# Kernel tuning notes

Hardware: AMD Instinct MI355X
Metric: run time of the kernel (lower is better)

The kernel has to match this reference:

```python
import jax, jax.numpy as jnp
import numpy as np

B, N_REG, D_IN = 32, 116, 256
N_NODES = B * N_REG            # 3712
E_PER_G = N_REG * 10           # avg degree 10
E = B * E_PER_G                # 37120
HEADS = 8
HID = [256, 128, 64]
D_OUT = 256
LN_EPS = 1e-5


def _layer_norm(x, scale, bias):
    mu = x.mean(-1, keepdims=True)
    var = ((x - mu) ** 2).mean(-1, keepdims=True)
    return (x - mu) * jax.lax.rsqrt(var + LN_EPS) * scale + bias


def _gat_layer(x, W, b, a_src, a_dst, src, dst, concat):
    """PyG-style GATConv (shared lin, self-loops, leaky_relu 0.2) + ELU + LayerNorm."""
    N = x.shape[0]
    H, C = a_src.shape
    h = (x @ W).reshape(N, H, C)                      # (N, H, C)
    sl = jnp.arange(N, dtype=src.dtype)               # self-loops (PyG default)
    s = jnp.concatenate([src, sl])
    d = jnp.concatenate([dst, sl])
    al = (h * a_src).sum(-1)                          # (N, H)
    ar = (h * a_dst).sum(-1)                          # (N, H)
    e = jax.nn.leaky_relu(al[s] + ar[d], 0.2)         # (E', H)
    m = jax.ops.segment_max(e, d, num_segments=N)
    ex = jnp.exp(e - m[d])
    den = jax.ops.segment_sum(ex, d, num_segments=N)
    alpha = ex / den[d]                               # segment softmax over incoming edges
    out = jax.ops.segment_sum(h[s] * alpha[..., None], d, num_segments=N)  # (N, H, C)
    out = out.reshape(N, H * C) if concat else out.mean(1)
    return out + b


def setup_inputs() -> dict:
    key = jax.random.key(0)
    ks = list(jax.random.split(key, 32))
    node_features = jax.random.normal(ks[0], (N_NODES, D_IN), dtype=jnp.float32)
    # edges: random within each graph (disconnected batched graph)
    off = (jnp.arange(B, dtype=jnp.int32) * N_REG)[:, None]
    src = (jax.random.randint(ks[1], (B, E_PER_G), 0, N_REG, dtype=jnp.int32) + off).reshape(-1)
    dst = (jax.random.randint(ks[2], (B, E_PER_G), 0, N_REG, dtype=jnp.int32) + off).reshape(-1)
    batch = jnp.repeat(jnp.arange(B, dtype=jnp.int32), N_REG)

    def lin(k, fin, fout):
        s = 1.0 / np.sqrt(fin)
        return jax.random.uniform(k, (fin, fout), jnp.float32, -s, s)

    dims_in = [D_IN, HID[0] * HEADS, HID[1] * HEADS]
    p = {}
    ki = 3
    for i, (fin, c) in enumerate(zip(dims_in, HID)):
        concat = i < len(HID) - 1
        wdim = c * HEADS
        p[f"w{i}"] = lin(ks[ki], fin, wdim); ki += 1
        p[f"b{i}"] = jnp.zeros((wdim if concat else c,), jnp.float32)
        p[f"as{i}"] = jax.random.normal(ks[ki], (HEADS, c), jnp.float32) * 0.1; ki += 1
        p[f"ad{i}"] = jax.random.normal(ks[ki], (HEADS, c), jnp.float32) * 0.1; ki += 1
        ldim = wdim if concat else c
        p[f"ls{i}"] = jnp.ones((ldim,), jnp.float32)
        p[f"lb{i}"] = jnp.zeros((ldim,), jnp.float32)
    p["wp"] = lin(ks[ki], HID[-1], D_OUT); ki += 1
    p["bp"] = jnp.zeros((D_OUT,), jnp.float32)
    p["lsp"] = jnp.ones((D_OUT,), jnp.float32)
    p["lbp"] = jnp.zeros((D_OUT,), jnp.float32)
    p["wq"] = lin(ks[ki], D_OUT, 1); ki += 1
    p["bq"] = jnp.zeros((1,), jnp.float32)
    return dict(node_features=node_features, src=src, dst=dst, batch=batch, **p)


def reference(node_features, src, dst, batch,
              w0, b0, as0, ad0, ls0, lb0,
              w1, b1, as1, ad1, ls1, lb1,
              w2, b2, as2, ad2, ls2, lb2,
              wp, bp, lsp, lbp, wq, bq):
    x = node_features
    x = _layer_norm(jax.nn.elu(_gat_layer(x, w0, b0, as0, ad0, src, dst, True)), ls0, lb0)
    x = _layer_norm(jax.nn.elu(_gat_layer(x, w1, b1, as1, ad1, src, dst, True)), ls1, lb1)
    x = _layer_norm(jax.nn.elu(_gat_layer(x, w2, b2, as2, ad2, src, dst, False)), ls2, lb2)
    node_out = jax.nn.gelu(_layer_norm(x @ wp + bp, lsp, lbp), approximate=False)  # (N, 256)
    pool_w = jax.nn.softmax(node_out @ wq + bq, axis=0)                            # (N, 1) global softmax
    num = jax.ops.segment_sum(node_out * pool_w, batch, num_segments=B)            # (B, 256)
    den = jnp.maximum(jax.ops.segment_sum(pool_w, batch, num_segments=B), 1e-8)    # (B, 1)
    graph_features = num / den
    return graph_features, node_out
```

## Files before the change

kernel.cpp:

```cpp
#include <hip/hip_runtime.h>
#include <hip/hip_bf16.h>
#include <math.h>

typedef __hip_bfloat16 bf16;
typedef short short8 __attribute__((ext_vector_type(8)));
typedef float f32x4 __attribute__((ext_vector_type(4)));

__device__ __forceinline__ float b2f(const bf16 v) { return __bfloat162float(v); }
__device__ __forceinline__ bf16 f2b(const float v) { return __float2bfloat16(v); }

__device__ __forceinline__ float bits2f(short s) {
  unsigned u = ((unsigned)(unsigned short)s) << 16;
  float f;
  __builtin_memcpy(&f, &u, 4);
  return f;
}
__device__ __forceinline__ short f2bits(float f) {
  bf16 b = f2b(f);
  short s;
  __builtin_memcpy(&s, &b, 2);
  return s;
}

__device__ __forceinline__ float ldsel(const void* p, size_t i, int f32) {
  return f32 ? ((const float*)p)[i] : b2f(((const bf16*)p)[i]);
}
__device__ __forceinline__ void stsel(void* p, size_t i, float v, int f32) {
  if (f32) ((float*)p)[i] = v; else ((bf16*)p)[i] = f2b(v);
}

#define NN 3712
#define NE 37120
#define NG 32
#define NREG 116
#define MAXDEG 48

__global__ __launch_bounds__(256) void k_detect(const void* nf, const void* w0, int* flags) {
  __shared__ int bad[2];
  if (threadIdx.x < 2) bad[threadIdx.x] = 0;
  __syncthreads();
  const bf16* a = (const bf16*)nf;
  const bf16* b = (const bf16*)w0;
  int l0 = 0, l1 = 0;
  for (int i = threadIdx.x; i < 4096; i += 256) {
    float x = b2f(a[i]); if (!(fabsf(x) < 1e4f)) l0++;
    float y = b2f(b[i]); if (!(fabsf(y) < 1e4f)) l1++;
  }
  if (l0) atomicAdd(&bad[0], l0);
  if (l1) atomicAdd(&bad[1], l1);
  __syncthreads();
  if (threadIdx.x == 0) { flags[0] = bad[0] > 0; flags[1] = bad[1] > 0; }
}

__global__ __launch_bounds__(256) void k_zero(int* __restrict__ p, int n) {
  int i = blockIdx.x * 256 + threadIdx.x;
  if (i < n) p[i] = 0;
}

__global__ __launch_bounds__(256) void k_scatter(const int* __restrict__ src, const int* __restrict__ dst,
                                                 int* __restrict__ cnt, int* __restrict__ bucket, int E) {
  int e = blockIdx.x * 256 + threadIdx.x;
  if (e < E) {
    int d = dst[e], s = src[e];
    if ((unsigned)d < NN && (unsigned)s < NN) {
      int p = atomicAdd(&cnt[d], 1);
      if (p < MAXDEG) bucket[d * MAXDEG + p] = s;
    }
  }
}

__global__ __launch_bounds__(256) void k_tobf16(const void* __restrict__ in, bf16* __restrict__ out,
                                                int n, const int* __restrict__ flags, int fidx) {
  int f = flags[fidx];
  int i = blockIdx.x * 256 + threadIdx.x;
  if (i < n) out[i] = f2b(ldsel(in, i, f));
}

__global__ __launch_bounds__(256) void k_transpose(const void* __restrict__ W, bf16* __restrict__ Wt,
                                                   int K, int N, const int* __restrict__ flags) {
  int f = flags[1];
  __shared__ float tile[32][33];
  int tx = threadIdx.x & 31, ty = threadIdx.x >> 5;
  int k0 = blockIdx.x * 32, n0 = blockIdx.y * 32;
#pragma unroll
  for (int i = 0; i < 4; ++i)
    tile[ty + i * 8][tx] = ldsel(W, (size_t)(k0 + ty + i * 8) * N + n0 + tx, f);
  __syncthreads();
#pragma unroll
  for (int i = 0; i < 4; ++i)
    Wt[(size_t)(n0 + ty + i * 8) * K + k0 + tx] = f2b(tile[tx][ty + i * 8]);
}

__global__ __launch_bounds__(256) void k_gemm_mfma(const bf16* __restrict__ A, const bf16* __restrict__ Bt,
                                                   bf16* __restrict__ C, int M, int N, int K) {
  __shared__ short As[64 * 72];
  __shared__ short Bs[64 * 72];
  int tid = threadIdx.x;
  int wave = tid >> 6, lane = tid & 63;
  int wr = wave >> 1, wc = wave & 1;
  int quad = lane >> 4, ml = lane & 15;

  int nbx = N >> 6;
  int total = gridDim.x;
  int id = blockIdx.x;
  int tile = ((total & 7) == 0) ? ((id & 7) * (total >> 3) + (id >> 3)) : id;
  int n0 = (tile % nbx) << 6;
  int m0 = (tile / nbx) << 6;

  f32x4 acc[2][2];
#pragma unroll
  for (int rt = 0; rt < 2; ++rt)
#pragma unroll
    for (int ct = 0; ct < 2; ++ct)
#pragma unroll
      for (int r = 0; r < 4; ++r) acc[rt][ct][r] = 0.f;

  for (int k0 = 0; k0 < K; k0 += 64) {
    __syncthreads();
#pragma unroll
    for (int i = 0; i < 2; ++i) {
      int c = tid + (i << 8);
      int row = c >> 3, kg = (c & 7) << 3;
      *(uint4*)&As[row * 72 + kg] = *(const uint4*)&A[(size_t)(m0 + row) * K + k0 + kg];
      *(uint4*)&Bs[row * 72 + kg] = *(const uint4*)&Bt[(size_t)(n0 + row) * K + k0 + kg];
    }
    __syncthreads();
    short8 af[2][2], bfr[2][2];
#pragma unroll
    for (int rt = 0; rt < 2; ++rt)
#pragma unroll
      for (int kk = 0; kk < 2; ++kk)
        af[rt][kk] = *(const short8*)&As[(wr * 32 + rt * 16 + ml) * 72 + kk * 32 + quad * 8];
#pragma unroll
    for (int ct = 0; ct < 2; ++ct)
#pragma unroll
      for (int kk = 0; kk < 2; ++kk)
        bfr[ct][kk] = *(const short8*)&Bs[(wc * 32 + ct * 16 + ml) * 72 + kk * 32 + quad * 8];
#pragma unroll
    for (int rt = 0; rt < 2; ++rt)
#pragma unroll
      for (int ct = 0; ct < 2; ++ct)
#pragma unroll
        for (int kk = 0; kk < 2; ++kk)
          acc[rt][ct] = __builtin_amdgcn_mfma_f32_16x16x32_bf16(af[rt][kk], bfr[ct][kk], acc[rt][ct], 0, 0, 0);
  }
#pragma unroll
  for (int rt = 0; rt < 2; ++rt)
#pragma unroll
    for (int ct = 0; ct < 2; ++ct)
#pragma unroll
      for (int r = 0; r < 4; ++r) {
        int grow = m0 + wr * 32 + rt * 16 + quad * 4 + r;
        int gcol = n0 + wc * 32 + ct * 16 + ml;
        C[(size_t)grow * N + gcol] = f2b(acc[rt][ct][r]);
      }
}

__global__ __launch_bounds__(256) void k_attn(const bf16* __restrict__ H, const void* __restrict__ a_s,
                                              const void* __restrict__ a_d, float* __restrict__ al,
                                              float* __restrict__ ar, int C, const int* __restrict__ flags) {
  int wF = flags[1];
  int n = blockIdx.x;
  int t = threadIdx.x;
  int D = 8 * C;
  int i0 = t * 8;
  if (i0 >= D) return;
  union { short8 v; short s[8]; } u;
  u.v = *(const short8*)&H[(size_t)n * D + i0];
  float ps = 0.f, pd = 0.f;
#pragma unroll
  for (int j = 0; j < 8; ++j) {
    float h = bits2f(u.s[j]);
    ps = fmaf(h, ldsel(a_s, i0 + j, wF), ps);
    pd = fmaf(h, ldsel(a_d, i0 + j, wF), pd);
  }
  int G = C >> 3;
  for (int off = G >> 1; off; off >>= 1) {
    ps += __shfl_xor(ps, off);
    pd += __shfl_xor(pd, off);
  }
  if ((t & (G - 1)) == 0) {
    int hd = i0 / C;
    al[n * 8 + hd] = ps;
    ar[n * 8 + hd] = pd;
  }
}

__global__ void k_agg(const bf16* __restrict__ H, const float* __restrict__ al,
                      const float* __restrict__ ar, const int* __restrict__ cnt,
                      const int* __restrict__ bucket, const void* __restrict__ bias,
                      const void* __restrict__ ls, const void* __restrict__ lb,
                      bf16* __restrict__ Xout, int C, int concat,
                      const int* __restrict__ flags) {
  int wF = flags[1];
  int bid = blockIdx.x;
  int x = bid & 7, jj = bid >> 3;
  int d = (x + ((jj / NREG) << 3)) * NREG + (jj % NREG);
  int t = threadIdx.x;
  int nt = blockDim.x;
  int lane = t & 63, wave = t >> 6;
  int D = 8 * C;
  __shared__ int sid[MAXDEG + 8];
  __shared__ float w[8][MAXDEG + 8];
  __shared__ float vals[512];
  __shared__ float r1[4], r2[4];
  __shared__ float sMu, sRs;

  int deg = cnt[d]; deg = deg > MAXDEG ? MAXDEG : deg;
  int total = deg + 1;
  int padded = (total + 7) & ~7;
  if (t < deg) sid[t] = bucket[d * MAXDEG + t];
  else if (t < padded) sid[t] = d;
  __syncthreads();

  int i0 = t * 8;
  int hd = i0 / C;
  int G = C >> 3;
  int gl = t & (G - 1);
  float ard = ar[d * 8 + hd];
  float m = -1e30f;
  for (int e = gl; e < total; e += G) {
    float lg = al[sid[e] * 8 + hd] + ard;
    lg = lg > 0.f ? lg : 0.2f * lg;
    w[hd][e] = lg;
    m = fmaxf(m, lg);
  }
  for (int off = G >> 1; off; off >>= 1) m = fmaxf(m, __shfl_xor(m, off));
  float den = 0.f;
  for (int e = gl; e < total; e += G) { float xv = expf(w[hd][e] - m); w[hd][e] = xv; den += xv; }
  for (int off = G >> 1; off; off >>= 1) den += __shfl_xor(den, off);
  float inv = 1.f / den;
  for (int e = gl; e < total; e += G) w[hd][e] *= inv;
  if (gl < padded - total) w[hd][total + gl] = 0.f;

  float acc[8] = {0.f, 0.f, 0.f, 0.f, 0.f, 0.f, 0.f, 0.f};
  const bf16* __restrict__ Hp = H + i0;
  for (int eb = 0; eb < padded; eb += 8) {
    short8 u[8];
#pragma unroll
    for (int j = 0; j < 8; ++j)
      u[j] = *(const short8*)&Hp[(size_t)sid[eb + j] * D];
#pragma unroll
    for (int j = 0; j < 8; ++j) {
      float we = w[hd][eb + j];
      union { short8 v; short s[8]; } uu; uu.v = u[j];
#pragma unroll
      for (int k = 0; k < 8; ++k) acc[k] = fmaf(we, bits2f(uu.s[k]), acc[k]);
    }
  }

  if (concat) {
    float v[8];
    float s1 = 0.f, s2 = 0.f;
#pragma unroll
    for (int j = 0; j < 8; ++j) {
      float vv = acc[j] + ldsel(bias, i0 + j, wF);
      vv = vv > 0.f ? vv : expf(vv) - 1.f;
      v[j] = vv; s1 += vv; s2 += vv * vv;
    }
#pragma unroll
    for (int off = 32; off; off >>= 1) { s1 += __shfl_down(s1, off); s2 += __shfl_down(s2, off); }
    if (lane == 0) { r1[wave] = s1; r2[wave] = s2; }
    __syncthreads();
    if (t == 0) {
      float S1 = 0.f, S2 = 0.f;
      int nw = nt >> 6;
      for (int i = 0; i < nw; ++i) { S1 += r1[i]; S2 += r2[i]; }
      float mu = S1 / D;
      sMu = mu; sRs = rsqrtf(S2 / D - mu * mu + 1e-5f);
    }
    __syncthreads();
    union { short8 v; short s[8]; } ou;
#pragma unroll
    for (int j = 0; j < 8; ++j)
      ou.s[j] = f2bits((v[j] - sMu) * sRs * ldsel(ls, i0 + j, wF) + ldsel(lb, i0 + j, wF));
    *(short8*)&Xout[(size_t)d * D + i0] = ou.v;
  } else {
#pragma unroll
    for (int j = 0; j < 8; ++j) vals[i0 + j] = acc[j];
    __syncthreads();
    float v = 0.f;
#pragma unroll
    for (int h = 0; h < 8; ++h) v += vals[h * 64 + t];
    v = v * 0.125f + ldsel(bias, t, wF);
    v = v > 0.f ? v : expf(v) - 1.f;
    float s1 = v, s2 = v * v;
#pragma unroll
    for (int off = 32; off; off >>= 1) { s1 += __shfl_xor(s1, off); s2 += __shfl_xor(s2, off); }
    float mu = s1 * (1.f / 64.f);
    float var = s2 * (1.f / 64.f) - mu * mu;
    float rs = rsqrtf(var + 1e-5f);
    Xout[(size_t)d * 64 + t] = f2b((v - mu) * rs * ldsel(ls, t, wF) + ldsel(lb, t, wF));
  }
}

__global__ __launch_bounds__(256) void k_proj(const bf16* __restrict__ X3, const void* __restrict__ wp,
                                              const void* __restrict__ bp, const void* __restrict__ lsp,
                                              const void* __restrict__ lbp, const void* __restrict__ wq,
                                              const void* __restrict__ bq,
                                              float* __restrict__ q, void* __restrict__ dout,
                                              const int* __restrict__ flags) {
  int wF = flags[1], xF = flags[0];
  int n = blockIdx.x, t = threadIdx.x;
  int lane = t & 63, wave = t >> 6;
  __shared__ float xs[64];
  __shared__ float r1[4], r2[4];
  __shared__ float sMu, sRs;
  if (t < 64) xs[t] = b2f(X3[n * 64 + t]);
  __syncthreads();
  float y = ldsel(bp, t, wF);
#pragma unroll 8
  for (int k = 0; k < 64; ++k) y = fmaf(xs[k], ldsel(wp, k * 256 + t, wF), y);
  float s1 = y, s2 = y * y;
#pragma unroll
  for (int off = 32; off; off >>= 1) { s1 += __shfl_down(s1, off); s2 += __shfl_down(s2, off); }
  if (lane == 0) { r1[wave] = s1; r2[wave] = s2; }
  __syncthreads();
  if (t == 0) {
    float S1 = r1[0] + r1[1] + r1[2] + r1[3];
    float S2 = r2[0] + r2[1] + r2[2] + r2[3];
    float mu = S1 / 256.f;
    sMu = mu; sRs = rsqrtf(S2 / 256.f - mu * mu + 1e-5f);
  }
  __syncthreads();
  float v = (y - sMu) * sRs * ldsel(lsp, t, wF) + ldsel(lbp, t, wF);
  float g = 0.5f * v * (1.f + erff(v * 0.70710678118654752f));
  stsel(dout, (size_t)NG * 256 + (size_t)n * 256 + t, g, xF);
  float qv = g * ldsel(wq, t, wF);
#pragma unroll
  for (int off = 32; off; off >>= 1) qv += __shfl_down(qv, off);
  if (lane == 0) r1[wave] = qv;
  __syncthreads();
  if (t == 0) q[n] = r1[0] + r1[1] + r1[2] + r1[3] + ldsel(bq, 0, wF);
}

__global__ __launch_bounds__(256) void k_pool(void* __restrict__ dout, const float* __restrict__ q,
                                              const int* __restrict__ flags) {
  int xF = flags[0];
  int b = blockIdx.x, t = threadIdx.x;
  __shared__ float es[NREG];
  __shared__ float sDen;
  if (t < NREG) es[t] = q[b * NREG + t];
  __syncthreads();
  if (t == 0) {
    float m = -1e30f;
    for (int i = 0; i < NREG; ++i) m = fmaxf(m, es[i]);
    float den = 0.f;
    for (int i = 0; i < NREG; ++i) { float e = expf(es[i] - m); es[i] = e; den += e; }
    sDen = den;
  }
  __syncthreads();
  float acc = 0.f;
  for (int i = 0; i < NREG; ++i)
    acc = fmaf(es[i], ldsel(dout, (size_t)NG * 256 + (size_t)(b * NREG + i) * 256 + t, xF), acc);
  stsel(dout, (size_t)b * 256 + t, acc / sDen, xF);
}

extern "C" void kernel_launch(void* const* d_in, const int* in_sizes, int n_in,
                              void* d_out, int out_size, void* d_ws, size_t ws_size,
                              hipStream_t stream) {
  const void* nf  = d_in[0];
  const int* src  = (const int*)d_in[1];
  const int* dst  = (const int*)d_in[2];
  const void *w0 = d_in[4],  *b0 = d_in[5],  *as0 = d_in[6], *ad0 = d_in[7],  *ls0 = d_in[8],  *lb0 = d_in[9];
  const void *w1 = d_in[10], *b1 = d_in[11], *as1 = d_in[12], *ad1 = d_in[13], *ls1 = d_in[14], *lb1 = d_in[15];
  const void *w2 = d_in[16], *b2 = d_in[17], *as2 = d_in[18], *ad2 = d_in[19], *ls2 = d_in[20], *lb2 = d_in[21];
  const void *wp = d_in[22], *bp = d_in[23], *lsp = d_in[24], *lbp = d_in[25], *wq = d_in[26], *bq = d_in[27];

  int* flags  = (int*)d_ws;
  float* al   = (float*)(flags + 4);
  float* ar   = al + NN * 8;
  int* cnt    = (int*)(ar + NN * 8);
  int* bucket = cnt + NN;
  float* q    = (float*)(bucket + NN * MAXDEG);
  bf16* X     = (bf16*)(q + NN);
  bf16* Hb    = X + (size_t)NN * 2048;

  bf16* X0  = X;
  bf16* wt0 = X + (1 << 20);
  bf16* wt1 = Hb + (size_t)NN * 1024;
  bf16* wt2 = Hb + (size_t)NN * 512;

  k_detect<<<1, 256, 0, stream>>>(nf, w0, flags);
  k_zero<<<(NN + 255) / 256, 256, 0, stream>>>(cnt, NN);
  k_scatter<<<(NE + 255) / 256, 256, 0, stream>>>(src, dst, cnt, bucket, NE);
  k_tobf16<<<(NN * 256 + 255) / 256, 256, 0, stream>>>(nf, X0, NN * 256, flags, 0);

  k_transpose<<<dim3(256 / 32, 2048 / 32), 256, 0, stream>>>(w0, wt0, 256, 2048, flags);
  k_gemm_mfma<<<(2048 / 64) * (NN / 64), 256, 0, stream>>>(X0, wt0, Hb, NN, 2048, 256);
  k_attn<<<NN, 256, 0, stream>>>(Hb, as0, ad0, al, ar, 256, flags);
  k_agg<<<NN, 256, 0, stream>>>(Hb, al, ar, cnt, bucket, b0, ls0, lb0, X, 256, 1, flags);

  k_transpose<<<dim3(2048 / 32, 1024 / 32), 256, 0, stream>>>(w1, wt1, 2048, 1024, flags);
  k_gemm_mfma<<<(1024 / 64) * (NN / 64), 256, 0, stream>>>(X, wt1, Hb, NN, 1024, 2048);
  k_attn<<<NN, 128, 0, stream>>>(Hb, as1, ad1, al, ar, 128, flags);
  k_agg<<<NN, 128, 0, stream>>>(Hb, al, ar, cnt, bucket, b1, ls1, lb1, X, 128, 1, flags);

  k_transpose<<<dim3(1024 / 32, 512 / 32), 256, 0, stream>>>(w2, wt2, 1024, 512, flags);
  k_gemm_mfma<<<(512 / 64) * (NN / 64), 256, 0, stream>>>(X, wt2, Hb, NN, 512, 1024);
  k_attn<<<NN, 64, 0, stream>>>(Hb, as2, ad2, al, ar, 64, flags);
  k_agg<<<NN, 64, 0, stream>>>(Hb, al, ar, cnt, bucket, b2, ls2, lb2, X, 64, 0, flags);

  k_proj<<<NN, 256, 0, stream>>>(X, wp, bp, lsp, lbp, wq, bq, q, d_out, flags);
  k_pool<<<NG, 256, 0, stream>>>(d_out, q, flags);
}
```

Baseline: 386.2 us.

## Precompute per-node softmax max/denominator in separate kernel and recompute weights on the fly

Moves the segment-softmax max and denominator computation out of the aggregation kernel into a new k_edgew kernel that handles four destinations per block. The aggregation kernel now recomputes each edge weight inline from al/ar plus the stored max and inverse denominator, processing edges in groups of 4 and dropping the shared weight array. k_attn now handles 8 nodes per block with hoisted attention vectors. Separately, d_out is reused as scratch for the max and inverse buffers. The new kernel adds a launch per layer, and k_edgew assumes at most 56 edges per destination.

```diff
diff --git a/kernel.cpp b/kernel.cpp
--- a/kernel.cpp
+++ b/kernel.cpp
@@ -156,38 +156,76 @@
       }
 }
 
-__global__ __launch_bounds__(256) void k_attn(const bf16* __restrict__ H, const void* __restrict__ a_s,
-                                              const void* __restrict__ a_d, float* __restrict__ al,
-                                              float* __restrict__ ar, int C, const int* __restrict__ flags) {
+__global__ void k_attn(const bf16* __restrict__ H, const void* __restrict__ a_s,
+                       const void* __restrict__ a_d, float* __restrict__ al,
+                       float* __restrict__ ar, int C, const int* __restrict__ flags) {
   int wF = flags[1];
-  int n = blockIdx.x;
   int t = threadIdx.x;
   int D = 8 * C;
   int i0 = t * 8;
-  if (i0 >= D) return;
-  union { short8 v; short s[8]; } u;
-  u.v = *(const short8*)&H[(size_t)n * D + i0];
-  float ps = 0.f, pd = 0.f;
-#pragma unroll
-  for (int j = 0; j < 8; ++j) {
-    float h = bits2f(u.s[j]);
-    ps = fmaf(h, ldsel(a_s, i0 + j, wF), ps);
-    pd = fmaf(h, ldsel(a_d, i0 + j, wF), pd);
-  }
+  float as8[8], ad8[8];
+#pragma unroll
+  for (int j = 0; j < 8; ++j) { as8[j] = ldsel(a_s, i0 + j, wF); ad8[j] = ldsel(a_d, i0 + j, wF); }
   int G = C >> 3;
-  for (int off = G >> 1; off; off >>= 1) {
-    ps += __shfl_xor(ps, off);
-    pd += __shfl_xor(pd, off);
-  }
-  if ((t & (G - 1)) == 0) {
-    int hd = i0 / C;
-    al[n * 8 + hd] = ps;
-    ar[n * 8 + hd] = pd;
-  }
+  int hd = i0 / C;
+  for (int it = 0; it < 8; ++it) {
+    int n = blockIdx.x * 8 + it;
+    union { short8 v; short s[8]; } u;
+    u.v = *(const short8*)&H[(size_t)n * D + i0];
+    float ps = 0.f, pd = 0.f;
+#pragma unroll
+    for (int j = 0; j < 8; ++j) {
+      float h = bits2f(u.s[j]);
+      ps = fmaf(h, as8[j], ps);
+      pd = fmaf(h, ad8[j], pd);
+    }
+    for (int off = G >> 1; off; off >>= 1) {
+      ps += __shfl_xor(ps, off);
+      pd += __shfl_xor(pd, off);
+    }
+    if ((t & (G - 1)) == 0) {
+      al[n * 8 + hd] = ps;
+      ar[n * 8 + hd] = pd;
+    }
+  }
+}
+
+__global__ __launch_bounds__(256) void k_edgew(const float* __restrict__ al, const float* __restrict__ ar,
+                                               const int* __restrict__ cnt, const int* __restrict__ bucket,
+                                               float* __restrict__ mbuf, float* __restrict__ ibuf) {
+  int t = threadIdx.x;
+  int q = t >> 6, l = t & 63, hd = l >> 3, el = l & 7;
+  int d = blockIdx.x * 4 + q;
+  int deg = cnt[d]; deg = deg > MAXDEG ? MAXDEG : deg;
+  int total = deg + 1;
+  float ard = ar[d * 8 + hd];
+  float lgv[7];
+  float m = -1e30f;
+#pragma unroll
+  for (int k = 0; k < 7; ++k) {
+    int e = el + k * 8;
+    float lg = -1e30f;
+    if (e < total) {
+      int s = e < deg ? bucket[d * MAXDEG + e] : d;
+      lg = al[s * 8 + hd] + ard;
+      lg = lg > 0.f ? lg : 0.2f * lg;
+    }
+    lgv[k] = lg;
+    m = fmaxf(m, lg);
+  }
+#pragma unroll
+  for (int off = 4; off; off >>= 1) m = fmaxf(m, __shfl_xor(m, off));
+  float den = 0.f;
+#pragma unroll
+  for (int k = 0; k < 7; ++k) den += (lgv[k] > -1e29f) ? expf(lgv[k] - m) : 0.f;
+#pragma unroll
+  for (int off = 4; off; off >>= 1) den += __shfl_xor(den, off);
+  if (el == 0) { mbuf[d * 8 + hd] = m; ibuf[d * 8 + hd] = 1.f / den; }
 }
 
 __global__ void k_agg(const bf16* __restrict__ H, const float* __restrict__ al,
-                      const float* __restrict__ ar, const int* __restrict__ cnt,
+                      const float* __restrict__ ar, const float* __restrict__ mbuf,
+                      const float* __restrict__ ibuf, const int* __restrict__ cnt,
                       const int* __restrict__ bucket, const void* __restrict__ bias,
                       const void* __restrict__ ls, const void* __restrict__ lb,
                       bf16* __restrict__ Xout, int C, int concat,
@@ -200,52 +238,40 @@
   int nt = blockDim.x;
   int lane = t & 63, wave = t >> 6;
   int D = 8 * C;
-  __shared__ int sid[MAXDEG + 8];
-  __shared__ float w[8][MAXDEG + 8];
+  __shared__ int sid[MAXDEG + 4];
   __shared__ float vals[512];
   __shared__ float r1[4], r2[4];
   __shared__ float sMu, sRs;
 
   int deg = cnt[d]; deg = deg > MAXDEG ? MAXDEG : deg;
   int total = deg + 1;
-  int padded = (total + 7) & ~7;
-  if (t < deg) sid[t] = bucket[d * MAXDEG + t];
-  else if (t < padded) sid[t] = d;
+  int padded = (total + 3) & ~3;
+  if (t < padded) sid[t] = t < deg ? bucket[d * MAXDEG + t] : d;
   __syncthreads();
 
   int i0 = t * 8;
   int hd = i0 / C;
-  int G = C >> 3;
-  int gl = t & (G - 1);
-  float ard = ar[d * 8 + hd];
-  float m = -1e30f;
-  for (int e = gl; e < total; e += G) {
-    float lg = al[sid[e] * 8 + hd] + ard;
-    lg = lg > 0.f ? lg : 0.2f * lg;
-    w[hd][e] = lg;
-    m = fmaxf(m, lg);
-  }
-  for (int off = G >> 1; off; off >>= 1) m = fmaxf(m, __shfl_xor(m, off));
-  float den = 0.f;
-  for (int e = gl; e < total; e += G) { float xv = expf(w[hd][e] - m); w[hd][e] = xv; den += xv; }
-  for (int off = G >> 1; off; off >>= 1) den += __shfl_xor(den, off);
-  float inv = 1.f / den;
-  for (int e = gl; e < total; e += G) w[hd][e] *= inv;
-  if (gl < padded - total) w[hd][total + gl] = 0.f;
+  float m = mbuf[d * 8 + hd], inv = ibuf[d * 8 + hd], ard = ar[d * 8 + hd];
 
   float acc[8] = {0.f, 0.f, 0.f, 0.f, 0.f, 0.f, 0.f, 0.f};
   const bf16* __restrict__ Hp = H + i0;
-  for (int eb = 0; eb < padded; eb += 8) {
-    short8 u[8];
-#pragma unroll
-    for (int j = 0; j < 8; ++j)
-      u[j] = *(const short8*)&Hp[(size_t)sid[eb + j] * D];
-#pragma unroll
-    for (int j = 0; j < 8; ++j) {
-      float we = w[hd][eb + j];
-      union { short8 v; short s[8]; } uu; uu.v = u[j];
-#pragma unroll
-      for (int k = 0; k < 8; ++k) acc[k] = fmaf(we, bits2f(uu.s[k]), acc[k]);
+  for (int eb = 0; eb < padded; eb += 4) {
+    int s4[4]; float a4[4]; short8 u4[4];
+#pragma unroll
+    for (int j = 0; j < 4; ++j) s4[j] = sid[eb + j];
+#pragma unroll
+    for (int j = 0; j < 4; ++j) {
+      a4[j] = al[s4[j] * 8 + hd];
+      u4[j] = *(const short8*)&Hp[(size_t)s4[j] * D];
+    }
+#pragma unroll
+    for (int j = 0; j < 4; ++j) {
+      float lg = a4[j] + ard;
+      lg = lg > 0.f ? lg : 0.2f * lg;
+      float we = (eb + j) < total ? expf(lg - m) * inv : 0.f;
+      union { short8 v; short s[8]; } uu; uu.v = u4[j];
+#pragma unroll
+      for (int k2 = 0; k2 < 8; ++k2) acc[k2] = fmaf(we, bits2f(uu.s[k2]), acc[k2]);
     }
   }
 
@@ -376,6 +402,9 @@
   bf16* X     = (bf16*)(q + NN);
   bf16* Hb    = X + (size_t)NN * 2048;
 
+  float* mbuf = (float*)d_out;
+  float* ibuf = mbuf + NN * 8;
+
   bf16* X0  = X;
   bf16* wt0 = X + (1 << 20);
   bf16* wt1 = Hb + (size_t)NN * 1024;
@@ -388,18 +417,21 @@
 
   k_transpose<<<dim3(256 / 32, 2048 / 32), 256, 0, stream>>>(w0, wt0, 256, 2048, flags);
   k_gemm_mfma<<<(2048 / 64) * (NN / 64), 256, 0, stream>>>(X0, wt0, Hb, NN, 2048, 256);
-  k_attn<<<NN, 256, 0, stream>>>(Hb, as0, ad0, al, ar, 256, flags);
-  k_agg<<<NN, 256, 0, stream>>>(Hb, al, ar, cnt, bucket, b0, ls0, lb0, X, 256, 1, flags);
+  k_attn<<<NN / 8, 256, 0, stream>>>(Hb, as0, ad0, al, ar, 256, flags);
+  k_edgew<<<NN / 4, 256, 0, stream>>>(al, ar, cnt, bucket, mbuf, ibuf);
+  k_agg<<<NN, 256, 0, stream>>>(Hb, al, ar, mbuf, ibuf, cnt, bucket, b0, ls0, lb0, X, 256, 1, flags);
 
   k_transpose<<<dim3(2048 / 32, 1024 / 32), 256, 0, stream>>>(w1, wt1, 2048, 1024, flags);
   k_gemm_mfma<<<(1024 / 64) * (NN / 64), 256, 0, stream>>>(X, wt1, Hb, NN, 1024, 2048);
-  k_attn<<<NN, 128, 0, stream>>>(Hb, as1, ad1, al, ar, 128, flags);
-  k_agg<<<NN, 128, 0, stream>>>(Hb, al, ar, cnt, bucket, b1, ls1, lb1, X, 128, 1, flags);
+  k_attn<<<NN / 8, 128, 0, stream>>>(Hb, as1, ad1, al, ar, 128, flags);
+  k_edgew<<<NN / 4, 256, 0, stream>>>(al, ar, cnt, bucket, mbuf, ibuf);
+  k_agg<<<NN, 128, 0, stream>>>(Hb, al, ar, mbuf, ibuf, cnt, bucket, b1, ls1, lb1, X, 128, 1, flags);
 
   k_transpose<<<dim3(1024 / 32, 512 / 32), 256, 0, stream>>>(w2, wt2, 1024, 512, flags);
   k_gemm_mfma<<<(512 / 64) * (NN / 64), 256, 0, stream>>>(X, wt2, Hb, NN, 512, 1024);
-  k_attn<<<NN, 64, 0, stream>>>(Hb, as2, ad2, al, ar, 64, flags);
-  k_agg<<<NN, 64, 0, stream>>>(Hb, al, ar, cnt, bucket, b2, ls2, lb2, X, 64, 0, flags);
+  k_attn<<<NN / 8, 64, 0, stream>>>(Hb, as2, ad2, al, ar, 64, flags);
+  k_edgew<<<NN / 4, 256, 0, stream>>>(al, ar, cnt, bucket, mbuf, ibuf);
+  k_agg<<<NN, 64, 0, stream>>>(Hb, al, ar, mbuf, ibuf, cnt, bucket, b2, ls2, lb2, X, 64, 0, flags);
 
   k_proj<<<NN, 256, 0, stream>>>(X, wp, bp, lsp, lbp, wq, bq, q, d_out, flags);
   k_pool<<<NG, 256, 0, stream>>>(d_out, q, flags);
```

New measurement: 366.8 us. 5.0% less time.
